# Performance work log

Measured on AMD Instinct MI355X. Metric: run time of the kernel, lower is better.

Reference implementation:

```python
import jax, jax.numpy as jnp
import numpy as np

N = 100_000; E = 3_200_000; F = 128; HID = 64; L = 4; H = 4; HD = 16; EMB = 64


def _ln(x, g, b):
    m = x.mean(-1, keepdims=True)
    v = ((x - m) ** 2).mean(-1, keepdims=True)
    return (x - m) / jnp.sqrt(v + 1e-5) * g + b


def _gelu(x):
    return jax.nn.gelu(x, approximate=False)


def _gat(h, src, dst, invalid, Wl, al, Wo):
    # Wl: (H, HID, HD), al: (H, 2*HD), Wo: (H*HD, HID)
    hh = jnp.einsum('nf,hfd->hnd', h, Wl)          # (H, N, HD)
    hs = hh[:, src]                                 # (H, E, HD) gather
    hd = hh[:, dst]                                 # (H, E, HD) gather
    e = jnp.einsum('hed,hd->he', hs, al[:, :HD]) + jnp.einsum('hed,hd->he', hd, al[:, HD:])
    e = jnp.where(e >= 0, e, 0.2 * e)               # LeakyReLU(0.2)
    e = jnp.where(invalid[None, :], -jnp.inf, e)
    seg_max = jax.vmap(lambda v: jax.ops.segment_max(v, dst, num_segments=N))(e)
    seg_max = jnp.where(jnp.isfinite(seg_max), seg_max, 0.0)  # empty segments -> 0 (matches include_self=False init 0)
    alpha = jnp.exp(jnp.minimum(e - seg_max[:, dst], 20.0))
    alpha = jnp.where(invalid[None, :], 0.0, alpha)
    asum = jax.vmap(lambda v: jax.ops.segment_sum(v, dst, num_segments=N))(alpha)
    an = alpha / (asum[:, dst] + 1e-8)
    msg = an[..., None] * hs                        # (H, E, HD)
    agg = jax.vmap(lambda m: jax.ops.segment_sum(m, dst, num_segments=N))(msg)  # (H, N, HD)
    return agg.transpose(1, 0, 2).reshape(N, H * HD) @ Wo


def setup_inputs() -> dict:
    key = jax.random.key(0)
    ks = jax.random.split(key, 20)
    rn = lambda k, shape, s: jax.random.normal(k, shape, jnp.float32) * s
    return {
        'node_features': jax.random.normal(ks[0], (N, F), jnp.float32),
        'edge_index': jax.random.randint(ks[1], (2, E), 0, N),
        'mask': jnp.ones((N,), bool),
        'ln_in_g': jnp.ones((F,), jnp.float32), 'ln_in_b': jnp.zeros((F,), jnp.float32),
        'W_in': rn(ks[2], (F, HID), 0.08), 'b_in': jnp.zeros((HID,), jnp.float32),
        'Wg': rn(ks[3], (L, H, HID, HD), 0.12),
        'attn': rn(ks[4], (L, H, 2 * HD), 0.2),
        'Wout': rn(ks[5], (L, H * HD, HID), 0.12),
        'norm_g': jnp.ones((L, HID), jnp.float32), 'norm_b': jnp.zeros((L, HID), jnp.float32),
        'We1': rn(ks[6], (HID, HID), 0.12), 'be1': jnp.zeros((HID,), jnp.float32),
        'We2': rn(ks[7], (HID, EMB), 0.12), 'be2': jnp.zeros((EMB,), jnp.float32),
        'Wrp': rn(ks[8], (HID, HID // 2), 0.12), 'brp': jnp.zeros((HID // 2,), jnp.float32),
        'Wro': rn(ks[9], (HID // 2, 1), 0.15), 'bro': jnp.zeros((1,), jnp.float32),
        'Wrs': rn(ks[10], (HID, 1), 0.12),
    }


def reference(node_features, edge_index, mask, ln_in_g, ln_in_b, W_in, b_in, Wg, attn, Wout,
              norm_g, norm_b, We1, be1, We2, be2, Wrp, brp, Wro, bro, Wrs):
    src, dst = edge_index[0], edge_index[1]
    invalid = ~mask[src]
    # input projection (dropout = eval identity)
    h = _gelu(_ln(node_features, ln_in_g, ln_in_b) @ W_in + b_in)
    for l in range(L):
        h = _ln(h + _gat(h, src, dst, invalid, Wg[l], attn[l], Wout[l]), norm_g[l], norm_b[l])
    hv = h  # mask is all-True so h[mask] == h (static shape)
    emb = jnp.tanh(_gelu(hv @ We1 + be1) @ We2 + be2)
    proj = _gelu(hv @ Wrp + brp)
    pred = (proj @ Wro + bro + hv @ Wrs)[:, 0]
    return pred, emb
```

## Files before the change

### kernel.cpp

```cpp
#include <hip/hip_runtime.h>
#include <hip/hip_bf16.h>
#include <hip/hip_fp16.h>
#include <math.h>

#define N_NODES 100000
#define E_EDGES 3200000
#define NQUADS  25000
#define LAYERS  4
#define NBKT    782
#define NB1     512
#define CHUNK1  6250

__device__ __forceinline__ float gelu_f(float x) {
    return 0.5f * x * (1.0f + erff(x * 0.70710678118654752f));
}
__device__ __forceinline__ float dot4(float4 a, float4 b) {
    return a.x * b.x + a.y * b.y + a.z * b.z + a.w * b.w;
}
__device__ __forceinline__ float4 fma4(float s, float4 w, float4 a) {
    a.x += s * w.x; a.y += s * w.y; a.z += s * w.z; a.w += s * w.w;
    return a;
}


__global__ __launch_bounds__(1024) void k_hist1(const int* __restrict__ dst,
        int* __restrict__ counts1) {
    __shared__ int hcnt[NBKT];
    int b = blockIdx.x;
    int lo = b * CHUNK1, hi = min(E_EDGES, lo + CHUNK1);
    for (int j = threadIdx.x; j < NBKT; j += 1024) hcnt[j] = 0;
    __syncthreads();
    for (int i = lo + (int)threadIdx.x; i < hi; i += 1024)
        atomicAdd(&hcnt[dst[i] >> 7], 1);
    __syncthreads();
    int* out = counts1 + (size_t)b * NBKT;
    for (int j = threadIdx.x; j < NBKT; j += 1024) out[j] = hcnt[j];
}

__global__ __launch_bounds__(NB1) void k_cscan(int* __restrict__ counts1,
        int* __restrict__ cdeg) {
    __shared__ int wsum[NB1 / 64];
    int bucket = blockIdx.x;
    int tid = threadIdx.x, lane = tid & 63, w = tid >> 6;
    int v = counts1[(size_t)tid * NBKT + bucket];
    int x = v;
    #pragma unroll
    for (int s = 1; s < 64; s <<= 1) {
        int t = __shfl_up(x, s, 64);
        if (lane >= s) x += t;
    }
    if (lane == 63) wsum[w] = x;
    __syncthreads();
    int woff = 0;
    for (int i = 0; i < w; ++i) woff += wsum[i];
    x += woff;
    counts1[(size_t)tid * NBKT + bucket] = x - v;
    if (tid == NB1 - 1) cdeg[bucket] = x;
}

__global__ __launch_bounds__(1024) void k_cstart(const int* __restrict__ cdeg,
        int* __restrict__ cstart, int* __restrict__ off) {
    __shared__ int wsum[16];
    int tid = threadIdx.x, lane = tid & 63, w = tid >> 6;
    int v = (tid < NBKT) ? cdeg[tid] : 0;
    int x = v;
    #pragma unroll
    for (int s = 1; s < 64; s <<= 1) {
        int t = __shfl_up(x, s, 64);
        if (lane >= s) x += t;
    }
    if (lane == 63) wsum[w] = x;
    __syncthreads();
    int woff = 0;
    for (int i = 0; i < w; ++i) woff += wsum[i];
    x += woff;
    if (tid < NBKT) cstart[tid] = x - v;
    if (tid == 0) off[N_NODES] = E_EDGES;
}

__global__ __launch_bounds__(1024) void k_scatter1(const int* __restrict__ src,
        const int* __restrict__ dst, const int* __restrict__ cstart,
        const int* __restrict__ counts1, int* __restrict__ tmp) {
    __shared__ int hcnt[NBKT];
    int b = blockIdx.x;
    int lo = b * CHUNK1, hi = min(E_EDGES, lo + CHUNK1);
    const int* myoff = counts1 + (size_t)b * NBKT;
    for (int j = threadIdx.x; j < NBKT; j += 1024) hcnt[j] = 0;
    __syncthreads();
    for (int i = lo + (int)threadIdx.x; i < hi; i += 1024) {
        int s = src[i], d = dst[i];
        int bkt = d >> 7;
        int lr = atomicAdd(&hcnt[bkt], 1);
        int pos = cstart[bkt] + myoff[bkt] + lr;
        tmp[pos] = (s << 7) | (d & 127);
    }
}

__global__ __launch_bounds__(1024) void k_sort2(const int* __restrict__ tmp,
        const int* __restrict__ cstart, const int* __restrict__ cdeg,
        int* __restrict__ off, int* __restrict__ csr_src) {
    __shared__ int hist[128];
    __shared__ int cur[128];
    __shared__ int wsum0;
    int k = blockIdx.x;
    int tid = threadIdx.x;
    int base = cstart[k], m = cdeg[k];
    if (tid < 128) hist[tid] = 0;
    __syncthreads();
    for (int i = tid; i < m; i += 1024)
        atomicAdd(&hist[tmp[base + i] & 127], 1);
    __syncthreads();
    int v = 0, x = 0;
    if (tid < 128) { v = hist[tid]; x = v; }
    if (tid < 128) {
        int lane = tid & 63;
        #pragma unroll
        for (int s = 1; s < 64; s <<= 1) {
            int t = __shfl_up(x, s, 64);
            if (lane >= s) x += t;
        }
    }
    if (tid == 63) wsum0 = x;
    __syncthreads();
    if (tid < 128) {
        int excl = x - v + ((tid >= 64) ? wsum0 : 0);
        cur[tid] = excl;
        int node = k * 128 + tid;
        if (node < N_NODES) off[node] = base + excl;
    }
    __syncthreads();
    for (int i = tid; i < m; i += 1024) {
        int e = tmp[base + i];
        int r = atomicAdd(&cur[e & 127], 1);
        csr_src[base + r] = e >> 7;
    }
}


__global__ __launch_bounds__(256) void k_input_tr(const float4* __restrict__ x4,
        const float4* __restrict__ g4, const float4* __restrict__ b4,
        const float4* __restrict__ Win4, const float4* __restrict__ bin4,
        float4* __restrict__ h4,
        const float* __restrict__ Wg, const float4* __restrict__ al4,
        __half* __restrict__ hh, float* __restrict__ ssrc, float* __restrict__ sdst) {
    __shared__ float4 WL[128 * 16];
    __shared__ float4 WG[64 * 16];
    __shared__ float4 gb[64];
    __shared__ float4 binL[16];
    __shared__ float4 aL[32];
    __shared__ float4 hLw[4][4][33];
    for (int j = threadIdx.x; j < 2048; j += 256) WL[j] = Win4[j];
    for (int j = threadIdx.x; j < 4096; j += 256) {
        int h_ = j >> 10, rem = j & 1023;
        int k = rem >> 4, d = rem & 15;
        ((float*)WG)[k * 64 + h_ * 16 + d] = Wg[j];
    }
    if (threadIdx.x < 32) gb[threadIdx.x] = g4[threadIdx.x];
    else if (threadIdx.x < 64) gb[threadIdx.x] = b4[threadIdx.x - 32];
    else if (threadIdx.x < 80) binL[threadIdx.x - 64] = bin4[threadIdx.x - 64];
    else if (threadIdx.x < 112) aL[threadIdx.x - 80] = al4[threadIdx.x - 80];
    __syncthreads();
    int lane = threadIdx.x & 63, wid = threadIdx.x >> 6;
    int c = lane & 15, n = lane >> 4;
    int head = c >> 2, q = c & 3;
    float4 aA = aL[head * 8 + q];
    float4 aB = aL[head * 8 + 4 + q];
    int gw = blockIdx.x * 4 + wid, nw = gridDim.x * 4;
    for (int quad = gw; quad < NQUADS; quad += nw) {
        int node = quad * 4 + n;
        float4 xa = x4[(size_t)node * 32 + c];
        float4 xb = x4[(size_t)node * 32 + 16 + c];
        float s = xa.x + xa.y + xa.z + xa.w + xb.x + xb.y + xb.z + xb.w;
        #pragma unroll
        for (int m = 8; m >= 1; m >>= 1) s += __shfl_xor(s, m, 64);
        float mean = s * (1.0f / 128.0f);
        float4 da = make_float4(xa.x - mean, xa.y - mean, xa.z - mean, xa.w - mean);
        float4 db = make_float4(xb.x - mean, xb.y - mean, xb.z - mean, xb.w - mean);
        float v = dot4(da, da) + dot4(db, db);
        #pragma unroll
        for (int m = 8; m >= 1; m >>= 1) v += __shfl_xor(v, m, 64);
        float rstd = rsqrtf(v * (1.0f / 128.0f) + 1e-5f);
        float4 ga = gb[c], gc = gb[c + 16], ba = gb[32 + c], bc = gb[48 + c];
        float4 na = make_float4(da.x * rstd * ga.x + ba.x, da.y * rstd * ga.y + ba.y,
                                da.z * rstd * ga.z + ba.z, da.w * rstd * ga.w + ba.w);
        float4 nb = make_float4(db.x * rstd * gc.x + bc.x, db.y * rstd * gc.y + bc.y,
                                db.z * rstd * gc.z + bc.z, db.w * rstd * gc.w + bc.w);
        hLw[wid][n][c] = na;
        hLw[wid][n][c + 16] = nb;
        float4 acc = binL[c];
        #pragma unroll 4
        for (int k4 = 0; k4 < 32; ++k4) {
            float4 xq = hLw[wid][n][k4];
            float4 w0 = WL[(k4 * 4 + 0) * 16 + c];
            float4 w1 = WL[(k4 * 4 + 1) * 16 + c];
            float4 w2 = WL[(k4 * 4 + 2) * 16 + c];
            float4 w3 = WL[(k4 * 4 + 3) * 16 + c];
            acc = fma4(xq.x, w0, acc);
            acc = fma4(xq.y, w1, acc);
            acc = fma4(xq.z, w2, acc);
            acc = fma4(xq.w, w3, acc);
        }
        float4 o = make_float4(gelu_f(acc.x), gelu_f(acc.y), gelu_f(acc.z), gelu_f(acc.w));
        h4[(size_t)quad * 64 + lane] = o;
        hLw[wid][n][c] = o;
        float4 acc2 = make_float4(0.f, 0.f, 0.f, 0.f);
        #pragma unroll 4
        for (int k4 = 0; k4 < 16; ++k4) {
            float4 xq = hLw[wid][n][k4];
            float4 w0 = WG[(k4 * 4 + 0) * 16 + c];
            float4 w1 = WG[(k4 * 4 + 1) * 16 + c];
            float4 w2 = WG[(k4 * 4 + 2) * 16 + c];
            float4 w3 = WG[(k4 * 4 + 3) * 16 + c];
            acc2 = fma4(xq.x, w0, acc2);
            acc2 = fma4(xq.y, w1, acc2);
            acc2 = fma4(xq.z, w2, acc2);
            acc2 = fma4(xq.w, w3, acc2);
        }
        __half2 lo = __floats2half2_rn(acc2.x, acc2.y);
        __half2 hi = __floats2half2_rn(acc2.z, acc2.w);
        uint2 pk = make_uint2(*(unsigned*)&lo, *(unsigned*)&hi);
        *(uint2*)(hh + (size_t)node * 64 + 4 * c) = pk;
        float t1 = dot4(acc2, aA);
        float t2 = dot4(acc2, aB);
        t1 += __shfl_xor(t1, 1, 64); t1 += __shfl_xor(t1, 2, 64);
        t2 += __shfl_xor(t2, 1, 64); t2 += __shfl_xor(t2, 2, 64);
        if (q == 0) {
            ssrc[node * 4 + head] = t1;
            sdst[node * 4 + head] = t2;
        }
    }
}


__device__ __forceinline__ float4 wsum4(float4 v) {
    #pragma unroll
    for (int m = 32; m >= 1; m >>= 1) {
        v.x += __shfl_xor(v.x, m, 64);
        v.y += __shfl_xor(v.y, m, 64);
        v.z += __shfl_xor(v.z, m, 64);
        v.w += __shfl_xor(v.w, m, 64);
    }
    return v;
}
__device__ __forceinline__ float sel4(float4 v, int hd) {
    float r = v.x;
    if (hd == 1) r = v.y;
    if (hd == 2) r = v.z;
    if (hd == 3) r = v.w;
    return r;
}
__device__ __forceinline__ float4 pexp4(float4 s, float4 d) {
    float ex = s.x + d.x, ey = s.y + d.y, ez = s.z + d.z, ew = s.w + d.w;
    ex = (ex >= 0.f) ? ex : 0.2f * ex;
    ey = (ey >= 0.f) ? ey : 0.2f * ey;
    ez = (ez >= 0.f) ? ez : 0.2f * ez;
    ew = (ew >= 0.f) ? ew : 0.2f * ew;
    return make_float4(__expf(fminf(ex, 11.f)), __expf(fminf(ey, 11.f)),
                       __expf(fminf(ez, 11.f)), __expf(fminf(ew, 11.f)));
}
__device__ __forceinline__ void acc8(float w, uint4 hv,
        float& a0, float& a1, float& a2, float& a3,
        float& a4, float& a5, float& a6, float& a7) {
    float2 f0 = __half22float2(*(__half2*)&hv.x);
    float2 f1 = __half22float2(*(__half2*)&hv.y);
    float2 f2 = __half22float2(*(__half2*)&hv.z);
    float2 f3 = __half22float2(*(__half2*)&hv.w);
    a0 += w * f0.x; a1 += w * f0.y; a2 += w * f1.x; a3 += w * f1.y;
    a4 += w * f2.x; a5 += w * f2.y; a6 += w * f3.x; a7 += w * f3.y;
}

__global__ __launch_bounds__(256) void k_edge(const int* __restrict__ off,
        const int* __restrict__ csr_src, const float4* __restrict__ ssrc4,
        const float4* __restrict__ sdst4, const __half* __restrict__ hh,
        float4* __restrict__ agg4, int n) {
    __shared__ float pbuf[4][64][4];
    int lane = threadIdx.x & 63, wid = threadIdx.x >> 6;
    int sub = lane >> 3;
    int dp  = lane & 7;
    int hd2 = dp >> 1;
    const __half* hrow = hh + dp * 8;
    int gw = blockIdx.x * 4 + wid, nw = gridDim.x * 4;
    for (int node = gw; node < n; node += nw) {
        float4 sd = sdst4[node];
        int s0 = off[node], s1 = off[node + 1];
        if (s0 == s1) {
            if (sub == 0) {
                float4 z = make_float4(0.f, 0.f, 0.f, 0.f);
                agg4[(size_t)node * 16 + dp * 2]     = z;
                agg4[(size_t)node * 16 + dp * 2 + 1] = z;
            }
            continue;
        }
        float4 sum4 = make_float4(0.f, 0.f, 0.f, 0.f);
        float a0=0.f,a1=0.f,a2=0.f,a3=0.f,a4=0.f,a5=0.f,a6=0.f,a7=0.f;
        int idx = s0 + lane;
        int sn = 0;
        float4 p4 = make_float4(0.f, 0.f, 0.f, 0.f);
        if (idx < s1) {
            sn = csr_src[idx];
            p4 = pexp4(ssrc4[sn], sd);
        }
        for (int base = s0; base < s1; base += 64) {
            int cnt = min(64, s1 - base);
            int snc = sn;
            float4 p4c = p4;
            int nidx = base + 64 + lane;
            sn = 0;
            p4 = make_float4(0.f, 0.f, 0.f, 0.f);
            if (nidx < s1) {
                sn = csr_src[nidx];
                p4 = pexp4(ssrc4[sn], sd);
            }
            sum4.x += p4c.x; sum4.y += p4c.y; sum4.z += p4c.z; sum4.w += p4c.w;
            *(float4*)&pbuf[wid][lane][0] = p4c;
            int cnt8 = (cnt + 7) & ~7;
            int j = 0;
            for (; j + 32 <= cnt8; j += 32) {
                int eA = j + sub, eB = j + 8 + sub, eC = j + 16 + sub, eD = j + 24 + sub;
                int sA = __shfl(snc, eA, 64);
                int sB = __shfl(snc, eB, 64);
                int sC = __shfl(snc, eC, 64);
                int sD = __shfl(snc, eD, 64);
                uint4 hA = *(const uint4*)(hrow + (size_t)sA * 64);
                uint4 hB = *(const uint4*)(hrow + (size_t)sB * 64);
                uint4 hC = *(const uint4*)(hrow + (size_t)sC * 64);
                uint4 hD = *(const uint4*)(hrow + (size_t)sD * 64);
                float wA = pbuf[wid][eA][hd2];
                float wB = pbuf[wid][eB][hd2];
                float wC = pbuf[wid][eC][hd2];
                float wD = pbuf[wid][eD][hd2];
                acc8(wA, hA, a0,a1,a2,a3,a4,a5,a6,a7);
                acc8(wB, hB, a0,a1,a2,a3,a4,a5,a6,a7);
                acc8(wC, hC, a0,a1,a2,a3,a4,a5,a6,a7);
                acc8(wD, hD, a0,a1,a2,a3,a4,a5,a6,a7);
            }
            for (; j < cnt8; j += 8) {
                int eA = j + sub;
                int sA = __shfl(snc, eA, 64);
                float wA = pbuf[wid][eA][hd2];
                uint4 hA = *(const uint4*)(hrow + (size_t)sA * 64);
                acc8(wA, hA, a0,a1,a2,a3,a4,a5,a6,a7);
            }
        }
        float4 t = wsum4(sum4);
        float r0=a0,r1=a1,r2=a2,r3=a3,r4=a4,r5=a5,r6=a6,r7=a7;
        #pragma unroll
        for (int m = 8; m <= 32; m <<= 1) {
            r0 += __shfl_xor(r0, m, 64); r1 += __shfl_xor(r1, m, 64);
            r2 += __shfl_xor(r2, m, 64); r3 += __shfl_xor(r3, m, 64);
            r4 += __shfl_xor(r4, m, 64); r5 += __shfl_xor(r5, m, 64);
            r6 += __shfl_xor(r6, m, 64); r7 += __shfl_xor(r7, m, 64);
        }
        float inv = 1.0f / (sel4(t, hd2) + 1e-8f);
        if (sub == 0) {
            agg4[(size_t)node * 16 + dp * 2]     = make_float4(r0*inv, r1*inv, r2*inv, r3*inv);
            agg4[(size_t)node * 16 + dp * 2 + 1] = make_float4(r4*inv, r5*inv, r6*inv, r7*inv);
        }
    }
}


__global__ __launch_bounds__(256) void k_out_tr(const float4* __restrict__ agg4,
        const float4* __restrict__ Wout4, float4* __restrict__ h4,
        const float4* __restrict__ ng4, const float4* __restrict__ nb4_,
        const float* __restrict__ Wg, const float4* __restrict__ al4,
        __half* __restrict__ hh, float* __restrict__ ssrc, float* __restrict__ sdst) {
    __shared__ float4 WL[64 * 16];
    __shared__ float4 WG[64 * 16];
    __shared__ float4 gnb[32];
    __shared__ float4 aL[32];
    __shared__ float4 hLw[4][4][17];
    for (int j = threadIdx.x; j < 1024; j += 256) WL[j] = Wout4[j];
    for (int j = threadIdx.x; j < 4096; j += 256) {
        int h_ = j >> 10, rem = j & 1023;
        int k = rem >> 4, d = rem & 15;
        ((float*)WG)[k * 64 + h_ * 16 + d] = Wg[j];
    }
    if (threadIdx.x < 16) gnb[threadIdx.x] = ng4[threadIdx.x];
    else if (threadIdx.x < 32) gnb[threadIdx.x] = nb4_[threadIdx.x - 16];
    else if (threadIdx.x < 64) aL[threadIdx.x - 32] = al4[threadIdx.x - 32];
    __syncthreads();
    int lane = threadIdx.x & 63, wid = threadIdx.x >> 6;
    int c = lane & 15, n = lane >> 4;
    int head = c >> 2, q = c & 3;
    float4 gg = gnb[c], bb = gnb[16 + c];
    float4 aA = aL[head * 8 + q];
    float4 aB = aL[head * 8 + 4 + q];
    int gw = blockIdx.x * 4 + wid, nw = gridDim.x * 4;
    for (int quad = gw; quad < NQUADS; quad += nw) {
        int node = quad * 4 + n;
        hLw[wid][n][c] = agg4[(size_t)quad * 64 + lane];
        float4 acc = make_float4(0.f, 0.f, 0.f, 0.f);
        #pragma unroll 4
        for (int k4 = 0; k4 < 16; ++k4) {
            float4 xq = hLw[wid][n][k4];
            float4 w0 = WL[(k4 * 4 + 0) * 16 + c];
            float4 w1 = WL[(k4 * 4 + 1) * 16 + c];
            float4 w2 = WL[(k4 * 4 + 2) * 16 + c];
            float4 w3 = WL[(k4 * 4 + 3) * 16 + c];
            acc = fma4(xq.x, w0, acc);
            acc = fma4(xq.y, w1, acc);
            acc = fma4(xq.z, w2, acc);
            acc = fma4(xq.w, w3, acc);
        }
        float4 hv = h4[(size_t)quad * 64 + lane];
        float4 r = make_float4(acc.x + hv.x, acc.y + hv.y, acc.z + hv.z, acc.w + hv.w);
        float s = r.x + r.y + r.z + r.w;
        #pragma unroll
        for (int m = 8; m >= 1; m >>= 1) s += __shfl_xor(s, m, 64);
        float mean = s * (1.f / 64.f);
        float4 d = make_float4(r.x - mean, r.y - mean, r.z - mean, r.w - mean);
        float v = dot4(d, d);
        #pragma unroll
        for (int m = 8; m >= 1; m >>= 1) v += __shfl_xor(v, m, 64);
        float rstd = rsqrtf(v * (1.f / 64.f) + 1e-5f);
        float4 o = make_float4(d.x * rstd * gg.x + bb.x, d.y * rstd * gg.y + bb.y,
                               d.z * rstd * gg.z + bb.z, d.w * rstd * gg.w + bb.w);
        h4[(size_t)quad * 64 + lane] = o;
        hLw[wid][n][c] = o;
        float4 acc2 = make_float4(0.f, 0.f, 0.f, 0.f);
        #pragma unroll 4
        for (int k4 = 0; k4 < 16; ++k4) {
            float4 xq = hLw[wid][n][k4];
            float4 w0 = WG[(k4 * 4 + 0) * 16 + c];
            float4 w1 = WG[(k4 * 4 + 1) * 16 + c];
            float4 w2 = WG[(k4 * 4 + 2) * 16 + c];
            float4 w3 = WG[(k4 * 4 + 3) * 16 + c];
            acc2 = fma4(xq.x, w0, acc2);
            acc2 = fma4(xq.y, w1, acc2);
            acc2 = fma4(xq.z, w2, acc2);
            acc2 = fma4(xq.w, w3, acc2);
        }
        __half2 lo = __floats2half2_rn(acc2.x, acc2.y);
        __half2 hi = __floats2half2_rn(acc2.z, acc2.w);
        uint2 pk = make_uint2(*(unsigned*)&lo, *(unsigned*)&hi);
        *(uint2*)(hh + (size_t)node * 64 + 4 * c) = pk;
        float t1 = dot4(acc2, aA);
        float t2 = dot4(acc2, aB);
        t1 += __shfl_xor(t1, 1, 64); t1 += __shfl_xor(t1, 2, 64);
        t2 += __shfl_xor(t2, 1, 64); t2 += __shfl_xor(t2, 2, 64);
        if (q == 0) {
            ssrc[node * 4 + head] = t1;
            sdst[node * 4 + head] = t2;
        }
    }
}


__global__ __launch_bounds__(256) void k_out(const float4* __restrict__ agg4,
        const float4* __restrict__ Wout4, float4* __restrict__ h4,
        const float4* __restrict__ ng4, const float4* __restrict__ nb4_) {
    __shared__ float4 WL[64 * 16];
    __shared__ float4 gnb[32];
    __shared__ float4 hLw[4][4][17];
    for (int j = threadIdx.x; j < 1024; j += 256) WL[j] = Wout4[j];
    if (threadIdx.x < 16) gnb[threadIdx.x] = ng4[threadIdx.x];
    else if (threadIdx.x < 32) gnb[threadIdx.x] = nb4_[threadIdx.x - 16];
    __syncthreads();
    int lane = threadIdx.x & 63, wid = threadIdx.x >> 6;
    int c = lane & 15, n = lane >> 4;
    float4 gg = gnb[c], bb = gnb[16 + c];
    int gw = blockIdx.x * 4 + wid, nw = gridDim.x * 4;
    for (int quad = gw; quad < NQUADS; quad += nw) {
        hLw[wid][n][c] = agg4[(size_t)quad * 64 + lane];
        float4 acc = make_float4(0.f, 0.f, 0.f, 0.f);
        #pragma unroll 4
        for (int k4 = 0; k4 < 16; ++k4) {
            float4 xq = hLw[wid][n][k4];
            float4 w0 = WL[(k4 * 4 + 0) * 16 + c];
            float4 w1 = WL[(k4 * 4 + 1) * 16 + c];
            float4 w2 = WL[(k4 * 4 + 2) * 16 + c];
            float4 w3 = WL[(k4 * 4 + 3) * 16 + c];
            acc = fma4(xq.x, w0, acc);
            acc = fma4(xq.y, w1, acc);
            acc = fma4(xq.z, w2, acc);
            acc = fma4(xq.w, w3, acc);
        }
        float4 hv = h4[(size_t)quad * 64 + lane];
        float4 r = make_float4(acc.x + hv.x, acc.y + hv.y, acc.z + hv.z, acc.w + hv.w);
        float s = r.x + r.y + r.z + r.w;
        #pragma unroll
        for (int m = 8; m >= 1; m >>= 1) s += __shfl_xor(s, m, 64);
        float mean = s * (1.f / 64.f);
        float4 d = make_float4(r.x - mean, r.y - mean, r.z - mean, r.w - mean);
        float v = dot4(d, d);
        #pragma unroll
        for (int m = 8; m >= 1; m >>= 1) v += __shfl_xor(v, m, 64);
        float rstd = rsqrtf(v * (1.f / 64.f) + 1e-5f);
        float4 o = make_float4(d.x * rstd * gg.x + bb.x, d.y * rstd * gg.y + bb.y,
                               d.z * rstd * gg.z + bb.z, d.w * rstd * gg.w + bb.w);
        h4[(size_t)quad * 64 + lane] = o;
    }
}


__global__ __launch_bounds__(256) void k_final(const float4* __restrict__ h4,
        const float4* __restrict__ We1_4, const float4* __restrict__ be1_4,
        const float4* __restrict__ We2_4, const float4* __restrict__ be2_4,
        const float4* __restrict__ Wrp_4, const float4* __restrict__ brp_4,
        const float4* __restrict__ Wro_4, const float* __restrict__ bro,
        const float4* __restrict__ Wrs_4,
        float* __restrict__ pred, float4* __restrict__ emb4) {
    __shared__ float4 W1L[64 * 16], W2L[64 * 16], WPL[64 * 8];
    __shared__ float4 be1L[16], be2L[16], brpL[8], wroL[8], wrsL[16];
    __shared__ float broL;
    __shared__ float4 hLw[4][4][17], uLw[4][4][17];
    for (int j = threadIdx.x; j < 1024; j += 256) { W1L[j] = We1_4[j]; W2L[j] = We2_4[j]; }
    for (int j = threadIdx.x; j < 512; j += 256) WPL[j] = Wrp_4[j];
    if (threadIdx.x < 16) be1L[threadIdx.x] = be1_4[threadIdx.x];
    else if (threadIdx.x < 32) be2L[threadIdx.x - 16] = be2_4[threadIdx.x - 16];
    else if (threadIdx.x < 40) brpL[threadIdx.x - 32] = brp_4[threadIdx.x - 32];
    else if (threadIdx.x < 48) wroL[threadIdx.x - 40] = Wro_4[threadIdx.x - 40];
    else if (threadIdx.x < 64) wrsL[threadIdx.x - 48] = Wrs_4[threadIdx.x - 48];
    if (threadIdx.x == 64) broL = bro[0];
    __syncthreads();
    int lane = threadIdx.x & 63, wid = threadIdx.x >> 6;
    int c = lane & 15, n = lane >> 4;
    int gw = blockIdx.x * 4 + wid, nw = gridDim.x * 4;
    for (int quad = gw; quad < NQUADS; quad += nw) {
        float4 hv = h4[(size_t)quad * 64 + lane];
        hLw[wid][n][c] = hv;
        float4 acc = be1L[c];
        #pragma unroll 4
        for (int k4 = 0; k4 < 16; ++k4) {
            float4 xq = hLw[wid][n][k4];
            float4 w0 = W1L[(k4 * 4 + 0) * 16 + c];
            float4 w1 = W1L[(k4 * 4 + 1) * 16 + c];
            float4 w2 = W1L[(k4 * 4 + 2) * 16 + c];
            float4 w3 = W1L[(k4 * 4 + 3) * 16 + c];
            acc = fma4(xq.x, w0, acc);
            acc = fma4(xq.y, w1, acc);
            acc = fma4(xq.z, w2, acc);
            acc = fma4(xq.w, w3, acc);
        }
        float4 u = make_float4(gelu_f(acc.x), gelu_f(acc.y), gelu_f(acc.z), gelu_f(acc.w));
        uLw[wid][n][c] = u;
        float4 acc2 = be2L[c];
        #pragma unroll 4
        for (int k4 = 0; k4 < 16; ++k4) {
            float4 xq = uLw[wid][n][k4];
            float4 w0 = W2L[(k4 * 4 + 0) * 16 + c];
            float4 w1 = W2L[(k4 * 4 + 1) * 16 + c];
            float4 w2 = W2L[(k4 * 4 + 2) * 16 + c];
            float4 w3 = W2L[(k4 * 4 + 3) * 16 + c];
            acc2 = fma4(xq.x, w0, acc2);
            acc2 = fma4(xq.y, w1, acc2);
            acc2 = fma4(xq.z, w2, acc2);
            acc2 = fma4(xq.w, w3, acc2);
        }
        float4 e = make_float4(tanhf(acc2.x), tanhf(acc2.y), tanhf(acc2.z), tanhf(acc2.w));
        emb4[(size_t)quad * 64 + lane] = e;
        float contrib = dot4(hv, wrsL[c]);
        if (c < 8) {
            float4 a3 = brpL[c];
            #pragma unroll 4
            for (int k4 = 0; k4 < 16; ++k4) {
                float4 xq = hLw[wid][n][k4];
                float4 w0 = WPL[(k4 * 4 + 0) * 8 + c];
                float4 w1 = WPL[(k4 * 4 + 1) * 8 + c];
                float4 w2 = WPL[(k4 * 4 + 2) * 8 + c];
                float4 w3 = WPL[(k4 * 4 + 3) * 8 + c];
                a3 = fma4(xq.x, w0, a3);
                a3 = fma4(xq.y, w1, a3);
                a3 = fma4(xq.z, w2, a3);
                a3 = fma4(xq.w, w3, a3);
            }
            float4 p = make_float4(gelu_f(a3.x), gelu_f(a3.y), gelu_f(a3.z), gelu_f(a3.w));
            contrib += dot4(p, wroL[c]);
        }
        #pragma unroll
        for (int m = 8; m >= 1; m >>= 1) contrib += __shfl_xor(contrib, m, 64);
        if (c == 0) pred[quad * 4 + n] = contrib + broL;
    }
}


extern "C" void kernel_launch(void* const* d_in, const int* in_sizes, int n_in,
                              void* d_out, int out_size, void* d_ws, size_t ws_size,
                              hipStream_t stream) {
    const float* node_features = (const float*)d_in[0];
    const int*   edge_index    = (const int*)d_in[1];
    const float* ln_in_g = (const float*)d_in[3];
    const float* ln_in_b = (const float*)d_in[4];
    const float* W_in    = (const float*)d_in[5];
    const float* b_in    = (const float*)d_in[6];
    const float* Wg      = (const float*)d_in[7];
    const float* attn    = (const float*)d_in[8];
    const float* Wout    = (const float*)d_in[9];
    const float* norm_g  = (const float*)d_in[10];
    const float* norm_b  = (const float*)d_in[11];
    const float* We1     = (const float*)d_in[12];
    const float* be1     = (const float*)d_in[13];
    const float* We2     = (const float*)d_in[14];
    const float* be2     = (const float*)d_in[15];
    const float* Wrp     = (const float*)d_in[16];
    const float* brp     = (const float*)d_in[17];
    const float* Wro     = (const float*)d_in[18];
    const float* bro     = (const float*)d_in[19];
    const float* Wrs     = (const float*)d_in[20];

    const int* src = edge_index;
    const int* dst = edge_index + E_EDGES;

    char* ws = (char*)d_ws;
    size_t o = 0;
    auto alloc = [&](size_t bytes) {
        void* p = ws + o;
        o += (bytes + 255) & ~(size_t)255;
        return p;
    };
    int*    off     = (int*)alloc((size_t)(N_NODES + 1) * 4);
    int*    csr_src = (int*)alloc((size_t)E_EDGES * 4);
    float*  h       = (float*)alloc((size_t)N_NODES * 64 * 4);
    __half* hh      = (__half*)alloc((size_t)N_NODES * 64 * 2);
    float*  agg     = (float*)alloc((size_t)N_NODES * 64 * 4);
    float*  ssrc    = (float*)alloc((size_t)N_NODES * 4 * 4);
    float*  sdst    = (float*)alloc((size_t)N_NODES * 4 * 4);
    int*    counts1 = (int*)h;
    int*    cdeg    = counts1 + (size_t)NB1 * NBKT;
    int*    cstart  = cdeg + 1024;
    int*    tmp     = (int*)agg;

    float* pred = (float*)d_out;
    float* emb  = (float*)d_out + N_NODES;

    k_hist1<<<NB1, 1024, 0, stream>>>(dst, counts1);
    k_cscan<<<NBKT, NB1, 0, stream>>>(counts1, cdeg);
    k_cstart<<<1, 1024, 0, stream>>>(cdeg, cstart, off);
    k_scatter1<<<NB1, 1024, 0, stream>>>(src, dst, cstart, counts1, tmp);
    k_sort2<<<NBKT, 1024, 0, stream>>>(tmp, cstart, cdeg, off, csr_src);

    k_input_tr<<<768, 256, 0, stream>>>((const float4*)node_features, (const float4*)ln_in_g,
                                        (const float4*)ln_in_b, (const float4*)W_in,
                                        (const float4*)b_in, (float4*)h,
                                        Wg, (const float4*)attn, hh, ssrc, sdst);
    for (int l = 0; l < LAYERS; ++l) {
        k_edge<<<2048, 256, 0, stream>>>(off, csr_src, (const float4*)ssrc,
                                         (const float4*)sdst, hh, (float4*)agg, N_NODES);
        if (l < LAYERS - 1) {
            k_out_tr<<<1024, 256, 0, stream>>>((const float4*)agg,
                    (const float4*)(Wout + l * 4096), (float4*)h,
                    (const float4*)(norm_g + l * 64), (const float4*)(norm_b + l * 64),
                    Wg + (l + 1) * 4096, (const float4*)(attn + (l + 1) * 128),
                    hh, ssrc, sdst);
        } else {
            k_out<<<1024, 256, 0, stream>>>((const float4*)agg,
                    (const float4*)(Wout + l * 4096), (float4*)h,
                    (const float4*)(norm_g + l * 64), (const float4*)(norm_b + l * 64));
        }
    }
    k_final<<<768, 256, 0, stream>>>((const float4*)h, (const float4*)We1, (const float4*)be1,
                                     (const float4*)We2, (const float4*)be2,
                                     (const float4*)Wrp, (const float4*)brp,
                                     (const float4*)Wro, bro, (const float4*)Wrs,
                                     pred, (float4*)emb);
}
```

Baseline: 694.4 us.

## Fuse edge aggregation with output projection, layernorm and next-layer transform

Merges the per-layer edge aggregation kernel into the output-projection/layernorm/next-layer-transform kernel, so each wave aggregates four nodes into shared memory and then immediately applies Wout, the residual layernorm and the next layer's head projection. This removes the fp32 agg buffer round-trip through global memory and one launch per layer. Because the next layer's hh and attention scores are now written while other waves still read the current ones, the code ping-pongs between two sets of hh/ssrc/sdst buffers. The trade-offs are a larger fused kernel with more shared memory and registers, and fewer blocks (768/1280), which may cut occupancy for the latency-bound gather.

```diff
diff --git a/kernel.cpp b/kernel.cpp
--- a/kernel.cpp
+++ b/kernel.cpp
@@ -269,131 +269,124 @@
     a4 += w * f2.x; a5 += w * f2.y; a6 += w * f3.x; a7 += w * f3.y;
 }
 
-__global__ __launch_bounds__(256) void k_edge(const int* __restrict__ off,
+template<bool DO_TR>
+__global__ __launch_bounds__(256) void k_edge_tr(const int* __restrict__ off,
         const int* __restrict__ csr_src, const float4* __restrict__ ssrc4,
-        const float4* __restrict__ sdst4, const __half* __restrict__ hh,
-        float4* __restrict__ agg4, int n) {
-    __shared__ float pbuf[4][64][4];
-    int lane = threadIdx.x & 63, wid = threadIdx.x >> 6;
-    int sub = lane >> 3;
-    int dp  = lane & 7;
-    int hd2 = dp >> 1;
-    const __half* hrow = hh + dp * 8;
-    int gw = blockIdx.x * 4 + wid, nw = gridDim.x * 4;
-    for (int node = gw; node < n; node += nw) {
-        float4 sd = sdst4[node];
-        int s0 = off[node], s1 = off[node + 1];
-        if (s0 == s1) {
-            if (sub == 0) {
-                float4 z = make_float4(0.f, 0.f, 0.f, 0.f);
-                agg4[(size_t)node * 16 + dp * 2]     = z;
-                agg4[(size_t)node * 16 + dp * 2 + 1] = z;
-            }
-            continue;
-        }
-        float4 sum4 = make_float4(0.f, 0.f, 0.f, 0.f);
-        float a0=0.f,a1=0.f,a2=0.f,a3=0.f,a4=0.f,a5=0.f,a6=0.f,a7=0.f;
-        int idx = s0 + lane;
-        int sn = 0;
-        float4 p4 = make_float4(0.f, 0.f, 0.f, 0.f);
-        if (idx < s1) {
-            sn = csr_src[idx];
-            p4 = pexp4(ssrc4[sn], sd);
-        }
-        for (int base = s0; base < s1; base += 64) {
-            int cnt = min(64, s1 - base);
-            int snc = sn;
-            float4 p4c = p4;
-            int nidx = base + 64 + lane;
-            sn = 0;
-            p4 = make_float4(0.f, 0.f, 0.f, 0.f);
-            if (nidx < s1) {
-                sn = csr_src[nidx];
-                p4 = pexp4(ssrc4[sn], sd);
-            }
-            sum4.x += p4c.x; sum4.y += p4c.y; sum4.z += p4c.z; sum4.w += p4c.w;
-            *(float4*)&pbuf[wid][lane][0] = p4c;
-            int cnt8 = (cnt + 7) & ~7;
-            int j = 0;
-            for (; j + 32 <= cnt8; j += 32) {
-                int eA = j + sub, eB = j + 8 + sub, eC = j + 16 + sub, eD = j + 24 + sub;
-                int sA = __shfl(snc, eA, 64);
-                int sB = __shfl(snc, eB, 64);
-                int sC = __shfl(snc, eC, 64);
-                int sD = __shfl(snc, eD, 64);
-                uint4 hA = *(const uint4*)(hrow + (size_t)sA * 64);
-                uint4 hB = *(const uint4*)(hrow + (size_t)sB * 64);
-                uint4 hC = *(const uint4*)(hrow + (size_t)sC * 64);
-                uint4 hD = *(const uint4*)(hrow + (size_t)sD * 64);
-                float wA = pbuf[wid][eA][hd2];
-                float wB = pbuf[wid][eB][hd2];
-                float wC = pbuf[wid][eC][hd2];
-                float wD = pbuf[wid][eD][hd2];
-                acc8(wA, hA, a0,a1,a2,a3,a4,a5,a6,a7);
-                acc8(wB, hB, a0,a1,a2,a3,a4,a5,a6,a7);
-                acc8(wC, hC, a0,a1,a2,a3,a4,a5,a6,a7);
-                acc8(wD, hD, a0,a1,a2,a3,a4,a5,a6,a7);
-            }
-            for (; j < cnt8; j += 8) {
-                int eA = j + sub;
-                int sA = __shfl(snc, eA, 64);
-                float wA = pbuf[wid][eA][hd2];
-                uint4 hA = *(const uint4*)(hrow + (size_t)sA * 64);
-                acc8(wA, hA, a0,a1,a2,a3,a4,a5,a6,a7);
-            }
-        }
-        float4 t = wsum4(sum4);
-        float r0=a0,r1=a1,r2=a2,r3=a3,r4=a4,r5=a5,r6=a6,r7=a7;
-        #pragma unroll
-        for (int m = 8; m <= 32; m <<= 1) {
-            r0 += __shfl_xor(r0, m, 64); r1 += __shfl_xor(r1, m, 64);
-            r2 += __shfl_xor(r2, m, 64); r3 += __shfl_xor(r3, m, 64);
-            r4 += __shfl_xor(r4, m, 64); r5 += __shfl_xor(r5, m, 64);
-            r6 += __shfl_xor(r6, m, 64); r7 += __shfl_xor(r7, m, 64);
-        }
-        float inv = 1.0f / (sel4(t, hd2) + 1e-8f);
-        if (sub == 0) {
-            agg4[(size_t)node * 16 + dp * 2]     = make_float4(r0*inv, r1*inv, r2*inv, r3*inv);
-            agg4[(size_t)node * 16 + dp * 2 + 1] = make_float4(r4*inv, r5*inv, r6*inv, r7*inv);
-        }
-    }
-}
-
-
-__global__ __launch_bounds__(256) void k_out_tr(const float4* __restrict__ agg4,
+        const float4* __restrict__ sdst4, const __half* __restrict__ hh_in,
         const float4* __restrict__ Wout4, float4* __restrict__ h4,
         const float4* __restrict__ ng4, const float4* __restrict__ nb4_,
         const float* __restrict__ Wg, const float4* __restrict__ al4,
-        __half* __restrict__ hh, float* __restrict__ ssrc, float* __restrict__ sdst) {
+        __half* __restrict__ hh_out, float* __restrict__ ssrc_o,
+        float* __restrict__ sdst_o) {
     __shared__ float4 WL[64 * 16];
-    __shared__ float4 WG[64 * 16];
+    __shared__ float4 WG[DO_TR ? 64 * 16 : 1];
     __shared__ float4 gnb[32];
-    __shared__ float4 aL[32];
-    __shared__ float4 hLw[4][4][17];
+    __shared__ float4 aL[DO_TR ? 32 : 1];
+    __shared__ float  pbuf[4][64][4];
+    __shared__ float4 aggL[4][4][17];
     for (int j = threadIdx.x; j < 1024; j += 256) WL[j] = Wout4[j];
-    for (int j = threadIdx.x; j < 4096; j += 256) {
-        int h_ = j >> 10, rem = j & 1023;
-        int k = rem >> 4, d = rem & 15;
-        ((float*)WG)[k * 64 + h_ * 16 + d] = Wg[j];
+    if (DO_TR) {
+        for (int j = threadIdx.x; j < 4096; j += 256) {
+            int h_ = j >> 10, rem = j & 1023;
+            int k = rem >> 4, d = rem & 15;
+            ((float*)WG)[k * 64 + h_ * 16 + d] = Wg[j];
+        }
+        if (threadIdx.x >= 64 && threadIdx.x < 96) aL[threadIdx.x - 64] = al4[threadIdx.x - 64];
     }
     if (threadIdx.x < 16) gnb[threadIdx.x] = ng4[threadIdx.x];
     else if (threadIdx.x < 32) gnb[threadIdx.x] = nb4_[threadIdx.x - 16];
-    else if (threadIdx.x < 64) aL[threadIdx.x - 32] = al4[threadIdx.x - 32];
     __syncthreads();
     int lane = threadIdx.x & 63, wid = threadIdx.x >> 6;
-    int c = lane & 15, n = lane >> 4;
+    int sub = lane >> 3, dp = lane & 7, hd2 = dp >> 1;
+    const __half* hrow = hh_in + dp * 8;
+    int c = lane & 15, nn = lane >> 4;
     int head = c >> 2, q = c & 3;
     float4 gg = gnb[c], bb = gnb[16 + c];
-    float4 aA = aL[head * 8 + q];
-    float4 aB = aL[head * 8 + 4 + q];
+    float4 aA = make_float4(0, 0, 0, 0), aB = make_float4(0, 0, 0, 0);
+    if (DO_TR) { aA = aL[head * 8 + q]; aB = aL[head * 8 + 4 + q]; }
     int gw = blockIdx.x * 4 + wid, nw = gridDim.x * 4;
     for (int quad = gw; quad < NQUADS; quad += nw) {
-        int node = quad * 4 + n;
-        hLw[wid][n][c] = agg4[(size_t)quad * 64 + lane];
+        for (int t = 0; t < 4; ++t) {
+            int node = quad * 4 + t;
+            float4 sd = sdst4[node];
+            int s0 = off[node], s1 = off[node + 1];
+            if (s0 == s1) {
+                if (sub == 0) {
+                    float4 z = make_float4(0.f, 0.f, 0.f, 0.f);
+                    aggL[wid][t][dp * 2]     = z;
+                    aggL[wid][t][dp * 2 + 1] = z;
+                }
+                continue;
+            }
+            float4 sum4 = make_float4(0.f, 0.f, 0.f, 0.f);
+            float a0=0.f,a1=0.f,a2=0.f,a3=0.f,a4=0.f,a5=0.f,a6=0.f,a7=0.f;
+            int idx = s0 + lane;
+            int sn = 0;
+            float4 p4 = make_float4(0.f, 0.f, 0.f, 0.f);
+            if (idx < s1) {
+                sn = csr_src[idx];
+                p4 = pexp4(ssrc4[sn], sd);
+            }
+            for (int base = s0; base < s1; base += 64) {
+                int cnt = min(64, s1 - base);
+                int snc = sn;
+                float4 p4c = p4;
+                int nidx = base + 64 + lane;
+                sn = 0;
+                p4 = make_float4(0.f, 0.f, 0.f, 0.f);
+                if (nidx < s1) {
+                    sn = csr_src[nidx];
+                    p4 = pexp4(ssrc4[sn], sd);
+                }
+                sum4.x += p4c.x; sum4.y += p4c.y; sum4.z += p4c.z; sum4.w += p4c.w;
+                *(float4*)&pbuf[wid][lane][0] = p4c;
+                int cnt8 = (cnt + 7) & ~7;
+                int j = 0;
+                for (; j + 32 <= cnt8; j += 32) {
+                    int eA = j + sub, eB = j + 8 + sub, eC = j + 16 + sub, eD = j + 24 + sub;
+                    int sA = __shfl(snc, eA, 64);
+                    int sB = __shfl(snc, eB, 64);
+                    int sC = __shfl(snc, eC, 64);
+                    int sD = __shfl(snc, eD, 64);
+                    uint4 hA = *(const uint4*)(hrow + (size_t)sA * 64);
+                    uint4 hB = *(const uint4*)(hrow + (size_t)sB * 64);
+                    uint4 hC = *(const uint4*)(hrow + (size_t)sC * 64);
+                    uint4 hD = *(const uint4*)(hrow + (size_t)sD * 64);
+                    float wA = pbuf[wid][eA][hd2];
+                    float wB = pbuf[wid][eB][hd2];
+                    float wC = pbuf[wid][eC][hd2];
+                    float wD = pbuf[wid][eD][hd2];
+                    acc8(wA, hA, a0,a1,a2,a3,a4,a5,a6,a7);
+                    acc8(wB, hB, a0,a1,a2,a3,a4,a5,a6,a7);
+                    acc8(wC, hC, a0,a1,a2,a3,a4,a5,a6,a7);
+                    acc8(wD, hD, a0,a1,a2,a3,a4,a5,a6,a7);
+                }
+                for (; j < cnt8; j += 8) {
+                    int eA = j + sub;
+                    int sA = __shfl(snc, eA, 64);
+                    float wA = pbuf[wid][eA][hd2];
+                    uint4 hA = *(const uint4*)(hrow + (size_t)sA * 64);
+                    acc8(wA, hA, a0,a1,a2,a3,a4,a5,a6,a7);
+                }
+            }
+            float4 ts = wsum4(sum4);
+            #pragma unroll
+            for (int m = 8; m <= 32; m <<= 1) {
+                a0 += __shfl_xor(a0, m, 64); a1 += __shfl_xor(a1, m, 64);
+                a2 += __shfl_xor(a2, m, 64); a3 += __shfl_xor(a3, m, 64);
+                a4 += __shfl_xor(a4, m, 64); a5 += __shfl_xor(a5, m, 64);
+                a6 += __shfl_xor(a6, m, 64); a7 += __shfl_xor(a7, m, 64);
+            }
+            float inv = 1.0f / (sel4(ts, hd2) + 1e-8f);
+            if (sub == 0) {
+                aggL[wid][t][dp * 2]     = make_float4(a0*inv, a1*inv, a2*inv, a3*inv);
+                aggL[wid][t][dp * 2 + 1] = make_float4(a4*inv, a5*inv, a6*inv, a7*inv);
+            }
+        }
         float4 acc = make_float4(0.f, 0.f, 0.f, 0.f);
         #pragma unroll 4
         for (int k4 = 0; k4 < 16; ++k4) {
-            float4 xq = hLw[wid][n][k4];
+            float4 xq = aggL[wid][nn][k4];
             float4 w0 = WL[(k4 * 4 + 0) * 16 + c];
             float4 w1 = WL[(k4 * 4 + 1) * 16 + c];
             float4 w2 = WL[(k4 * 4 + 2) * 16 + c];
@@ -417,79 +410,35 @@
         float4 o = make_float4(d.x * rstd * gg.x + bb.x, d.y * rstd * gg.y + bb.y,
                                d.z * rstd * gg.z + bb.z, d.w * rstd * gg.w + bb.w);
         h4[(size_t)quad * 64 + lane] = o;
-        hLw[wid][n][c] = o;
-        float4 acc2 = make_float4(0.f, 0.f, 0.f, 0.f);
-        #pragma unroll 4
-        for (int k4 = 0; k4 < 16; ++k4) {
-            float4 xq = hLw[wid][n][k4];
-            float4 w0 = WG[(k4 * 4 + 0) * 16 + c];
-            float4 w1 = WG[(k4 * 4 + 1) * 16 + c];
-            float4 w2 = WG[(k4 * 4 + 2) * 16 + c];
-            float4 w3 = WG[(k4 * 4 + 3) * 16 + c];
-            acc2 = fma4(xq.x, w0, acc2);
-            acc2 = fma4(xq.y, w1, acc2);
-            acc2 = fma4(xq.z, w2, acc2);
-            acc2 = fma4(xq.w, w3, acc2);
-        }
-        __half2 lo = __floats2half2_rn(acc2.x, acc2.y);
-        __half2 hi = __floats2half2_rn(acc2.z, acc2.w);
-        uint2 pk = make_uint2(*(unsigned*)&lo, *(unsigned*)&hi);
-        *(uint2*)(hh + (size_t)node * 64 + 4 * c) = pk;
-        float t1 = dot4(acc2, aA);
-        float t2 = dot4(acc2, aB);
-        t1 += __shfl_xor(t1, 1, 64); t1 += __shfl_xor(t1, 2, 64);
-        t2 += __shfl_xor(t2, 1, 64); t2 += __shfl_xor(t2, 2, 64);
-        if (q == 0) {
-            ssrc[node * 4 + head] = t1;
-            sdst[node * 4 + head] = t2;
-        }
-    }
-}
-
-
-__global__ __launch_bounds__(256) void k_out(const float4* __restrict__ agg4,
-        const float4* __restrict__ Wout4, float4* __restrict__ h4,
-        const float4* __restrict__ ng4, const float4* __restrict__ nb4_) {
-    __shared__ float4 WL[64 * 16];
-    __shared__ float4 gnb[32];
-    __shared__ float4 hLw[4][4][17];
-    for (int j = threadIdx.x; j < 1024; j += 256) WL[j] = Wout4[j];
-    if (threadIdx.x < 16) gnb[threadIdx.x] = ng4[threadIdx.x];
-    else if (threadIdx.x < 32) gnb[threadIdx.x] = nb4_[threadIdx.x - 16];
-    __syncthreads();
-    int lane = threadIdx.x & 63, wid = threadIdx.x >> 6;
-    int c = lane & 15, n = lane >> 4;
-    float4 gg = gnb[c], bb = gnb[16 + c];
-    int gw = blockIdx.x * 4 + wid, nw = gridDim.x * 4;
-    for (int quad = gw; quad < NQUADS; quad += nw) {
-        hLw[wid][n][c] = agg4[(size_t)quad * 64 + lane];
-        float4 acc = make_float4(0.f, 0.f, 0.f, 0.f);
-        #pragma unroll 4
-        for (int k4 = 0; k4 < 16; ++k4) {
-            float4 xq = hLw[wid][n][k4];
-            float4 w0 = WL[(k4 * 4 + 0) * 16 + c];
-            float4 w1 = WL[(k4 * 4 + 1) * 16 + c];
-            float4 w2 = WL[(k4 * 4 + 2) * 16 + c];
-            float4 w3 = WL[(k4 * 4 + 3) * 16 + c];
-            acc = fma4(xq.x, w0, acc);
-            acc = fma4(xq.y, w1, acc);
-            acc = fma4(xq.z, w2, acc);
-            acc = fma4(xq.w, w3, acc);
-        }
-        float4 hv = h4[(size_t)quad * 64 + lane];
-        float4 r = make_float4(acc.x + hv.x, acc.y + hv.y, acc.z + hv.z, acc.w + hv.w);
-        float s = r.x + r.y + r.z + r.w;
-        #pragma unroll
-        for (int m = 8; m >= 1; m >>= 1) s += __shfl_xor(s, m, 64);
-        float mean = s * (1.f / 64.f);
-        float4 d = make_float4(r.x - mean, r.y - mean, r.z - mean, r.w - mean);
-        float v = dot4(d, d);
-        #pragma unroll
-        for (int m = 8; m >= 1; m >>= 1) v += __shfl_xor(v, m, 64);
-        float rstd = rsqrtf(v * (1.f / 64.f) + 1e-5f);
-        float4 o = make_float4(d.x * rstd * gg.x + bb.x, d.y * rstd * gg.y + bb.y,
-                               d.z * rstd * gg.z + bb.z, d.w * rstd * gg.w + bb.w);
-        h4[(size_t)quad * 64 + lane] = o;
+        if (DO_TR) {
+            int node = quad * 4 + nn;
+            aggL[wid][nn][c] = o;
+            float4 acc2 = make_float4(0.f, 0.f, 0.f, 0.f);
+            #pragma unroll 4
+            for (int k4 = 0; k4 < 16; ++k4) {
+                float4 xq = aggL[wid][nn][k4];
+                float4 w0 = WG[(k4 * 4 + 0) * 16 + c];
+                float4 w1 = WG[(k4 * 4 + 1) * 16 + c];
+                float4 w2 = WG[(k4 * 4 + 2) * 16 + c];
+                float4 w3 = WG[(k4 * 4 + 3) * 16 + c];
+                acc2 = fma4(xq.x, w0, acc2);
+                acc2 = fma4(xq.y, w1, acc2);
+                acc2 = fma4(xq.z, w2, acc2);
+                acc2 = fma4(xq.w, w3, acc2);
+            }
+            __half2 lo = __floats2half2_rn(acc2.x, acc2.y);
+            __half2 hi = __floats2half2_rn(acc2.z, acc2.w);
+            uint2 pk = make_uint2(*(unsigned*)&lo, *(unsigned*)&hi);
+            *(uint2*)(hh_out + (size_t)node * 64 + 4 * c) = pk;
+            float t1 = dot4(acc2, aA);
+            float t2 = dot4(acc2, aB);
+            t1 += __shfl_xor(t1, 1, 64); t1 += __shfl_xor(t1, 2, 64);
+            t2 += __shfl_xor(t2, 1, 64); t2 += __shfl_xor(t2, 2, 64);
+            if (q == 0) {
+                ssrc_o[node * 4 + head] = t1;
+                sdst_o[node * 4 + head] = t2;
+            }
+        }
     }
 }
 
@@ -612,14 +561,16 @@
     int*    off     = (int*)alloc((size_t)(N_NODES + 1) * 4);
     int*    csr_src = (int*)alloc((size_t)E_EDGES * 4);
     float*  h       = (float*)alloc((size_t)N_NODES * 64 * 4);
-    __half* hh      = (__half*)alloc((size_t)N_NODES * 64 * 2);
-    float*  agg     = (float*)alloc((size_t)N_NODES * 64 * 4);
-    float*  ssrc    = (float*)alloc((size_t)N_NODES * 4 * 4);
-    float*  sdst    = (float*)alloc((size_t)N_NODES * 4 * 4);
+    __half* hhA     = (__half*)alloc((size_t)N_NODES * 64 * 2);
+    __half* hhB     = (__half*)alloc((size_t)N_NODES * 64 * 2);
+    float*  ssrcA   = (float*)alloc((size_t)N_NODES * 4 * 4);
+    float*  ssrcB   = (float*)alloc((size_t)N_NODES * 4 * 4);
+    float*  sdstA   = (float*)alloc((size_t)N_NODES * 4 * 4);
+    float*  sdstB   = (float*)alloc((size_t)N_NODES * 4 * 4);
     int*    counts1 = (int*)h;
     int*    cdeg    = counts1 + (size_t)NB1 * NBKT;
     int*    cstart  = cdeg + 1024;
-    int*    tmp     = (int*)agg;
+    int*    tmp     = (int*)hhA;
 
     float* pred = (float*)d_out;
     float* emb  = (float*)d_out + N_NODES;
@@ -633,20 +584,26 @@
     k_input_tr<<<768, 256, 0, stream>>>((const float4*)node_features, (const float4*)ln_in_g,
                                         (const float4*)ln_in_b, (const float4*)W_in,
                                         (const float4*)b_in, (float4*)h,
-                                        Wg, (const float4*)attn, hh, ssrc, sdst);
+                                        Wg, (const float4*)attn, hhA, ssrcA, sdstA);
+
+    __half* hhs[2]  = { hhA, hhB };
+    float*  sss[2]  = { ssrcA, ssrcB };
+    float*  sds[2]  = { sdstA, sdstB };
     for (int l = 0; l < LAYERS; ++l) {
-        k_edge<<<2048, 256, 0, stream>>>(off, csr_src, (const float4*)ssrc,
-                                         (const float4*)sdst, hh, (float4*)agg, N_NODES);
+        int ib = l & 1, ob = ib ^ 1;
         if (l < LAYERS - 1) {
-            k_out_tr<<<1024, 256, 0, stream>>>((const float4*)agg,
+            k_edge_tr<true><<<768, 256, 0, stream>>>(off, csr_src,
+                    (const float4*)sss[ib], (const float4*)sds[ib], hhs[ib],
                     (const float4*)(Wout + l * 4096), (float4*)h,
                     (const float4*)(norm_g + l * 64), (const float4*)(norm_b + l * 64),
                     Wg + (l + 1) * 4096, (const float4*)(attn + (l + 1) * 128),
-                    hh, ssrc, sdst);
+                    hhs[ob], sss[ob], sds[ob]);
         } else {
-            k_out<<<1024, 256, 0, stream>>>((const float4*)agg,
+            k_edge_tr<false><<<1280, 256, 0, stream>>>(off, csr_src,
+                    (const float4*)sss[ib], (const float4*)sds[ib], hhs[ib],
                     (const float4*)(Wout + l * 4096), (float4*)h,
-                    (const float4*)(norm_g + l * 64), (const float4*)(norm_b + l * 64));
+                    (const float4*)(norm_g + l * 64), (const float4*)(norm_b + l * 64),
+                    Wg, (const float4*)attn, hhs[ob], sss[ob], sds[ob]);
         }
     }
     k_final<<<768, 256, 0, stream>>>((const float4*)h, (const float4*)We1, (const float4*)be1,
```

Result: slower. 728.8 us (+5.0%).
